# Kernel tuning notes

Measured on AMD Instinct MI355X. Metric: run time of the kernel, lower is better.

The kernel has to match this reference:

```python
import jax, jax.numpy as jnp
import numpy as np

B, N = 32, 512            # batch, max nodes per graph
F_DIM, M_DIM = 1024, 256  # node feature dim, first hidden dim
N_SEM = 8                 # number of semantic-class experts
XYZ, DIM_E = 3, 8
OUT_SIZE = 2 * XYZ + DIM_E  # 14 (default reg branch)
EPS = 1e-8                # padding value used by out_seq_to_batch


def setup_inputs() -> dict:
    key = jax.random.key(0)
    ks = jax.random.split(key, 12)
    def w(k, shape, fan_in):
        return jax.random.normal(k, shape, jnp.float32) / np.float32(np.sqrt(fan_in))
    return {
        "nodes": jax.random.normal(ks[0], (B, N, F_DIM), jnp.float32),
        "sem": jax.random.randint(ks[1], (B, N), 0, N_SEM, jnp.int32),
        "lengths": jax.random.randint(ks[2], (B,), 64, N + 1, jnp.int32),
        # y expert MLPs (4 layers), stacked over experts
        "W1": w(ks[3], (N_SEM, F_DIM, M_DIM), F_DIM), "b1": jnp.zeros((N_SEM, M_DIM), jnp.float32),
        "W2": w(ks[4], (N_SEM, M_DIM, 64), M_DIM),   "b2": jnp.zeros((N_SEM, 64), jnp.float32),
        "W3": w(ks[5], (N_SEM, 64, 32), 64),         "b3": jnp.zeros((N_SEM, 32), jnp.float32),
        "W4": w(ks[6], (N_SEM, 32, OUT_SIZE), 32),   "b4": jnp.zeros((N_SEM, OUT_SIZE), jnp.float32),
        # rot expert MLPs (2 layers), stacked over experts
        "R1": w(ks[7], (N_SEM, F_DIM, M_DIM), F_DIM), "rb1": jnp.zeros((N_SEM, M_DIM), jnp.float32),
        "R2": w(ks[8], (N_SEM, M_DIM, XYZ), M_DIM),   "rb2": jnp.zeros((N_SEM, XYZ), jnp.float32),
    }


def _prim_mlps(nodes, sem, lengths, W1, b1, W2, b2, W3, b3, W4, b4, R1, rb1, R2, rb2):
    Bn, Nn, Fd = nodes.shape
    x = nodes.reshape(-1, Fd)                       # [T, F], T = B*N tokens
    semf = sem.reshape(-1)                          # [T] expert id per token
    # dense dispatch: run every expert on all tokens, then select per token
    h1 = jax.nn.relu(jnp.einsum('tf,efm->etm', x, W1) + b1[:, None, :])   # [E,T,M]
    h2 = jax.nn.relu(jnp.einsum('etm,emh->eth', h1, W2) + b2[:, None, :]) # [E,T,64]
    h3 = jax.nn.relu(jnp.einsum('eth,ehg->etg', h2, W3) + b3[:, None, :]) # [E,T,32]
    y_all = jnp.einsum('etg,ego->eto', h3, W4) + b4[:, None, :]           # [E,T,OUT]
    r1 = jax.nn.relu(jnp.einsum('tf,efm->etm', x, R1) + rb1[:, None, :])  # [E,T,M]
    rot_all = jnp.einsum('etm,emo->eto', r1, R2) + rb2[:, None, :]        # [E,T,XYZ]
    t = jnp.arange(x.shape[0])
    y = y_all[semf, t]                              # [T, OUT]
    rot = rot_all[semf, t]                          # [T, XYZ]
    out = jnp.concatenate([y, rot], axis=-1).reshape(Bn, Nn, -1)
    # positions beyond each graph's length are filled with eps (out_seq_to_batch)
    mask = (jnp.arange(Nn)[None, :] < lengths[:, None])[:, :, None]
    return jnp.where(mask, out, jnp.float32(EPS))


def reference(nodes, sem, lengths, W1, b1, W2, b2, W3, b3, W4, b4, R1, rb1, R2, rb2):
    return _prim_mlps(nodes, sem, lengths, W1, b1, W2, b2, W3, b3, W4, b4,
                      R1, rb1, R2, rb2)
```

## Files before the change

kernel.cpp:

```cpp
#include <hip/hip_runtime.h>
#include <stdint.h>

#define T_TOK 16384
#define NE 8
#define EPSV 1e-8f
#define MAXC64  264
#define MAXC16  1032

#define WS_PERM   0
#define WS_PART   65536
#define WS_OFFS   67584
#define WS_XS     131072
#define WS_WT     (WS_XS + 16512*1024*2)
#define WS_H1     (WS_WT + 8*512*1024*2)
#define WS_W2T    (WS_H1 + 16448*512*2)
#define WS_W3T    (WS_W2T + 8*64*256*2)
#define WS_W4T    (WS_W3T + 8*32*64*2)
#define WS_R2T    (WS_W4T + 8*16*32*2)

typedef __attribute__((ext_vector_type(8))) short bf16x8;
typedef __attribute__((ext_vector_type(4))) float f32x4;

__device__ __forceinline__ unsigned short f2bf(float f) {
    unsigned u = __float_as_uint(f);
    u += 0x7fffu + ((u >> 16) & 1u);
    return (unsigned short)(u >> 16);
}

__device__ __forceinline__ void gl_lds16(const void* g, void* l) {
    __builtin_amdgcn_global_load_lds(
        (const __attribute__((address_space(1))) void*)g,
        (__attribute__((address_space(3))) void*)l,
        16, 0, 0);
}

__device__ __forceinline__ bool chunk_lookup(const int* __restrict__ offs, int c, int csize,
                                             int& e, int& base, int& len) {
    int acc = 0;
#pragma unroll
    for (int i = 0; i < NE; i++) {
        int s = offs[i], t = offs[i + 1];
        int cc = (t - s + csize - 1) / csize;
        if (c < acc + cc) {
            e = i;
            base = s + (c - acc) * csize;
            len = (t - base < csize) ? (t - base) : csize;
            return true;
        }
        acc += cc;
    }
    return false;
}

__global__ __launch_bounds__(256) void k_prep1(const float* __restrict__ W1,
                                               const float* __restrict__ R1,
                                               const float* __restrict__ W2,
                                               const float* __restrict__ W3,
                                               const float* __restrict__ W4,
                                               const float* __restrict__ R2,
                                               const int* __restrict__ sem,
                                               unsigned short* __restrict__ wt,
                                               unsigned short* __restrict__ w2t,
                                               unsigned short* __restrict__ w3t,
                                               unsigned short* __restrict__ w4t,
                                               unsigned short* __restrict__ r2t,
                                               int* __restrict__ ws_i) {
    __shared__ float tile[64][65];
    int id = blockIdx.x, tid = threadIdx.x;
    if (id >= 1024) {
        __shared__ int cnt[NE];
        int hb = id - 1024, lane = tid & 63;
        if (tid < NE) cnt[tid] = 0;
        __syncthreads();
        int s = sem[hb * 256 + tid];
#pragma unroll
        for (int e = 0; e < NE; e++) {
            unsigned long long m = __ballot(s == e);
            if (lane == e) atomicAdd(&cnt[e], (int)__popcll(m));
        }
        __syncthreads();
        if (tid < NE) ws_i[(WS_PART >> 2) + hb * NE + tid] = cnt[tid];
        return;
    }
    int e = id >> 7, rem = id & 127;
    int ny = rem >> 4, kx = rem & 15;
    int k0 = kx * 64, n0 = ny * 64;
    const float* src = (n0 < 256) ? (W1 + (size_t)e * 1024 * 256 + n0)
                                  : (R1 + (size_t)e * 1024 * 256 + (n0 - 256));
    int rr = tid >> 4;
    int cg = (tid & 15) * 4;
#pragma unroll
    for (int p = 0; p < 4; p++) {
        int kk = p * 16 + rr;
        float4 v = *(const float4*)(src + (size_t)(k0 + kk) * 256 + cg);
        tile[kk][cg] = v.x; tile[kk][cg + 1] = v.y; tile[kk][cg + 2] = v.z; tile[kk][cg + 3] = v.w;
    }
    __syncthreads();
    int nn = tid >> 3;
    int k8 = tid & 7;
#pragma unroll
    for (int p = 0; p < 2; p++) {
        int n = p * 32 + nn;
        unsigned w[4];
#pragma unroll
        for (int j = 0; j < 4; j++) {
            float f0 = tile[k8 * 8 + 2 * j][n];
            float f1 = tile[k8 * 8 + 2 * j + 1][n];
            w[j] = (unsigned)f2bf(f0) | ((unsigned)f2bf(f1) << 16);
        }
        *(uint4*)(wt + (size_t)(e * 512 + n0 + n) * 1024 + k0 + k8 * 8) =
            make_uint4(w[0], w[1], w[2], w[3]);
    }
    if (ny == 0) {
        int x = kx;
        for (int j = tid; j < 1024; j += 256) {
            int idx = x * 1024 + j; int k = idx & 255, n = idx >> 8;
            w2t[(size_t)(e * 64 + n) * 256 + k] = f2bf(W2[(size_t)e * 16384 + k * 64 + n]);
        }
        if (tid < 128) {
            int idx = x * 128 + tid; int k = idx & 63, n = idx >> 6;
            w3t[(size_t)(e * 32 + n) * 64 + k] = f2bf(W3[(size_t)e * 2048 + k * 32 + n]);
        }
        if (tid < 32) {
            int idx = x * 32 + tid; int k = idx & 31, n = idx >> 5;
            w4t[(size_t)(e * 16 + n) * 32 + k] = (n < 14) ? f2bf(W4[(size_t)e * 448 + k * 14 + n])
                                                          : (unsigned short)0;
        }
        {
            int idx = x * 256 + tid; int k = idx & 255, n = idx >> 8;
            r2t[(size_t)(e * 16 + n) * 256 + k] = (n < 3) ? f2bf(R2[(size_t)e * 768 + k * 3 + n])
                                                          : (unsigned short)0;
        }
    }
}

__global__ __launch_bounds__(256) void k_scatter(const int* __restrict__ sem,
                                                 const float* __restrict__ nodes,
                                                 int* __restrict__ ws_i,
                                                 unsigned short* __restrict__ xs) {
    __shared__ int parts[512];
    __shared__ int tot[NE], preb[NE], ebase[NE + 1];
    __shared__ int wcnt[4][NE];
    __shared__ int destS[256];
    int b = blockIdx.x, g = b >> 3, j = b & 7;
    int tid = threadIdx.x, wave = tid >> 6, lane = tid & 63;
    parts[tid] = ws_i[(WS_PART >> 2) + tid];
    parts[256 + tid] = ws_i[(WS_PART >> 2) + 256 + tid];
    __syncthreads();
    if (tid < NE) {
        int t = 0, p = 0;
        for (int bb = 0; bb < 64; bb++) {
            int v = parts[bb * NE + tid];
            t += v;
            if (bb < g) p += v;
        }
        tot[tid] = t; preb[tid] = p;
    }
    __syncthreads();
    if (tid == 0) {
        int base = 0;
        for (int e = 0; e < NE; e++) { ebase[e] = base; base += tot[e]; }
        ebase[NE] = base;
        if (b == 0)
            for (int e = 0; e <= NE; e++) ws_i[(WS_OFFS >> 2) + e] = ebase[e];
    }
    int i = g * 256 + tid;
    int s = sem[i];
    int rank = 0;
#pragma unroll
    for (int e = 0; e < NE; e++) {
        unsigned long long m = __ballot(s == e);
        if (s == e) rank = (int)__popcll(m & ((1ull << lane) - 1ull));
        if (lane == e) wcnt[wave][e] = (int)__popcll(m);
    }
    __syncthreads();
    int wpre = 0;
#pragma unroll
    for (int w = 0; w < 4; w++)
        if (w < wave) wpre += wcnt[w][s];
    int dest = ebase[s] + preb[s] + wpre + rank;
    destS[tid] = dest;
    if (j == 0) ws_i[(WS_PERM >> 2) + dest] = i;
    __syncthreads();
#pragma unroll 4
    for (int r = j * 32; r < j * 32 + 32; r++) {
        int tok = g * 256 + r;
        int d = destS[r];
        float4 v = *(const float4*)(nodes + (size_t)tok * 1024 + tid * 4);
        unsigned p0 = (unsigned)f2bf(v.x) | ((unsigned)f2bf(v.y) << 16);
        unsigned p1 = (unsigned)f2bf(v.z) | ((unsigned)f2bf(v.w) << 16);
        *(uint2*)(xs + (size_t)d * 1024 + tid * 4) = make_uint2(p0, p1);
    }
}

__global__ __launch_bounds__(256) void k_gemm(const unsigned short* __restrict__ xs,
                                              const unsigned short* __restrict__ wt,
                                              const float* __restrict__ b1,
                                              const float* __restrict__ rb1,
                                              const int* __restrict__ ws_i,
                                              unsigned short* __restrict__ h1) {
    __shared__ __align__(16) short As[2][64 * 64];
    __shared__ __align__(16) short Bs[2][128 * 64];
    int e, base, len;
    if (!chunk_lookup(ws_i + (WS_OFFS >> 2), blockIdx.x, 64, e, base, len)) return;
    int n0 = blockIdx.y * 128;
    int tid = threadIdx.x;
    int wave = tid >> 6, lane = tid & 63;
    int quad = lane >> 4, lr = lane & 15;
    int wn = wave * 32;

    f32x4 acc[4][2];
#pragma unroll
    for (int i = 0; i < 4; i++)
#pragma unroll
        for (int j = 0; j < 2; j++) acc[i][j] = (f32x4){0.f, 0.f, 0.f, 0.f};

    const unsigned short* Ag = xs + (size_t)base * 1024;
    const unsigned short* Bg = wt + (size_t)(e * 512 + n0) * 1024;

    const unsigned short* srcA[2];
    int dstA[2];
#pragma unroll
    for (int i = 0; i < 2; i++) {
        int s = i * 256 + wave * 64 + lane;
        int r = s >> 3, cs = (s & 7) ^ (r & 7);
        srcA[i] = Ag + (size_t)r * 1024 + cs * 8;
        dstA[i] = (i * 256 + wave * 64) * 8;
    }
    const unsigned short* srcB[4];
    int dstB[4];
#pragma unroll
    for (int i = 0; i < 4; i++) {
        int s = i * 256 + wave * 64 + lane;
        int r = s >> 3, cs = (s & 7) ^ (r & 7);
        srcB[i] = Bg + (size_t)r * 1024 + cs * 8;
        dstB[i] = (i * 256 + wave * 64) * 8;
    }

#pragma unroll
    for (int i = 0; i < 2; i++) gl_lds16(srcA[i], &As[0][dstA[i]]);
#pragma unroll
    for (int i = 0; i < 4; i++) gl_lds16(srcB[i], &Bs[0][dstB[i]]);

    for (int kb = 0; kb < 16; kb++) {
        int cur = kb & 1;
        if (kb < 15) {
            int nxt = cur ^ 1;
#pragma unroll
            for (int i = 0; i < 2; i++) gl_lds16(srcA[i] + (kb + 1) * 64, &As[nxt][dstA[i]]);
#pragma unroll
            for (int i = 0; i < 4; i++) gl_lds16(srcB[i] + (kb + 1) * 64, &Bs[nxt][dstB[i]]);
            asm volatile("s_waitcnt vmcnt(6)" ::: "memory");
        } else {
            asm volatile("s_waitcnt vmcnt(0)" ::: "memory");
        }
        __builtin_amdgcn_sched_barrier(0);
        __builtin_amdgcn_s_barrier();

        const short* Ab = As[cur];
        const short* Bb = Bs[cur];
        bf16x8 af[2][4], bfr[2][2];
#pragma unroll
        for (int im = 0; im < 4; im++) {
            int r = im * 16 + lr;
#pragma unroll
            for (int kh = 0; kh < 2; kh++) {
                int q = kh * 4 + quad;
                af[kh][im] = *(const bf16x8*)(Ab + (r * 8 + (q ^ (r & 7))) * 8);
            }
        }
#pragma unroll
        for (int in = 0; in < 2; in++) {
            int r = wn + in * 16 + lr;
#pragma unroll
            for (int kh = 0; kh < 2; kh++) {
                int q = kh * 4 + quad;
                bfr[kh][in] = *(const bf16x8*)(Bb + (r * 8 + (q ^ (r & 7))) * 8);
            }
        }
#pragma unroll
        for (int kh = 0; kh < 2; kh++)
#pragma unroll
            for (int im = 0; im < 4; im++)
#pragma unroll
                for (int in = 0; in < 2; in++)
                    acc[im][in] = __builtin_amdgcn_mfma_f32_16x16x32_bf16(af[kh][im], bfr[kh][in], acc[im][in], 0, 0, 0);

        if (kb < 15) {
            __builtin_amdgcn_sched_barrier(0);
            __builtin_amdgcn_s_barrier();
        }
    }

#pragma unroll
    for (int in = 0; in < 2; in++) {
        int gcol = n0 + wn + in * 16 + lr;
        float bias = (gcol < 256) ? b1[e * 256 + gcol] : rb1[e * 256 + gcol - 256];
#pragma unroll
        for (int im = 0; im < 4; im++) {
#pragma unroll
            for (int v = 0; v < 4; v++) {
                int r = im * 16 + quad * 4 + v;
                if (r < len) {
                    float val = fmaxf(acc[im][in][v] + bias, 0.f);
                    h1[(size_t)(base + r) * 512 + gcol] = f2bf(val);
                }
            }
        }
    }
}

__global__ __launch_bounds__(256) void k_tail(const unsigned short* __restrict__ h1,
                                              const int* __restrict__ ws_i,
                                              const unsigned short* __restrict__ w2t,
                                              const unsigned short* __restrict__ w3t,
                                              const unsigned short* __restrict__ w4t,
                                              const unsigned short* __restrict__ r2t,
                                              const float* __restrict__ b2,
                                              const float* __restrict__ b3,
                                              const float* __restrict__ b4,
                                              const float* __restrict__ rb2,
                                              const int* __restrict__ lengths,
                                              float* __restrict__ out) {
    __shared__ __align__(16) unsigned short h2s[16][64];
    __shared__ __align__(16) unsigned short h3s[16][32];

    int e, base, len;
    if (!chunk_lookup(ws_i + (WS_OFFS >> 2), blockIdx.x, 16, e, base, len)) return;
    int tid = threadIdx.x, wave = tid >> 6, lane = tid & 63;
    int quad = lane >> 4, lr = lane & 15;
    int lead = blockIdx.x & 3;

    const unsigned short* Ap = h1 + (size_t)base * 512;

    f32x4 acc2;
    { float bb = b2[e * 64 + wave * 16 + lr]; acc2 = (f32x4){bb, bb, bb, bb}; }
    f32x4 accr;
    { float bb = (lr < 3) ? rb2[e * 3 + lr] : 0.f; accr = (f32x4){bb, bb, bb, bb}; }

    const unsigned short* W2e = w2t + (size_t)e * 64 * 256;
    const unsigned short* R2e = r2t + (size_t)e * 16 * 256;
#pragma unroll
    for (int kk = 0; kk < 8; kk++) {
        int k0 = kk * 32;
        bf16x8 a = *(const bf16x8*)(Ap + lr * 512 + k0 + quad * 8);
        bf16x8 b = *(const bf16x8*)(W2e + (wave * 16 + lr) * 256 + k0 + quad * 8);
        acc2 = __builtin_amdgcn_mfma_f32_16x16x32_bf16(a, b, acc2, 0, 0, 0);
        if (wave == lead) {
            bf16x8 ar = *(const bf16x8*)(Ap + lr * 512 + 256 + k0 + quad * 8);
            bf16x8 br = *(const bf16x8*)(R2e + lr * 256 + k0 + quad * 8);
            accr = __builtin_amdgcn_mfma_f32_16x16x32_bf16(ar, br, accr, 0, 0, 0);
        }
    }
#pragma unroll
    for (int v = 0; v < 4; v++)
        h2s[quad * 4 + v][wave * 16 + lr] = f2bf(fmaxf(acc2[v], 0.f));
    __syncthreads();
    if (wave != lead) return;

    f32x4 acc3[2];
#pragma unroll
    for (int t = 0; t < 2; t++) {
        float bb = b3[e * 32 + t * 16 + lr];
        acc3[t] = (f32x4){bb, bb, bb, bb};
    }
    const unsigned short* W3e = w3t + (size_t)e * 32 * 64;
#pragma unroll
    for (int kk = 0; kk < 2; kk++) {
        int k0 = kk * 32;
        bf16x8 a = *(const bf16x8*)(&h2s[lr][k0 + quad * 8]);
#pragma unroll
        for (int t = 0; t < 2; t++) {
            bf16x8 b = *(const bf16x8*)(W3e + (t * 16 + lr) * 64 + k0 + quad * 8);
            acc3[t] = __builtin_amdgcn_mfma_f32_16x16x32_bf16(a, b, acc3[t], 0, 0, 0);
        }
    }
#pragma unroll
    for (int t = 0; t < 2; t++)
#pragma unroll
        for (int v = 0; v < 4; v++)
            h3s[quad * 4 + v][t * 16 + lr] = f2bf(fmaxf(acc3[t][v], 0.f));

    f32x4 acc4;
    { float bb = (lr < 14) ? b4[e * 14 + lr] : 0.f; acc4 = (f32x4){bb, bb, bb, bb}; }
    {
        bf16x8 a = *(const bf16x8*)(&h3s[lr][quad * 8]);
        bf16x8 b = *(const bf16x8*)(w4t + ((size_t)e * 16 + lr) * 32 + quad * 8);
        acc4 = __builtin_amdgcn_mfma_f32_16x16x32_bf16(a, b, acc4, 0, 0, 0);
    }

    const int* perm = ws_i + (WS_PERM >> 2);
#pragma unroll
    for (int v = 0; v < 4; v++) {
        int t = quad * 4 + v;
        if (t < len) {
            int token = perm[base + t];
            int bi = token >> 9, ni = token & 511;
            int valid = ni < lengths[bi];
            if (lr < 14) out[(size_t)token * 17 + lr] = valid ? acc4[v] : EPSV;
            if (lr < 3)  out[(size_t)token * 17 + 14 + lr] = valid ? accr[v] : EPSV;
        }
    }
}

extern "C" void kernel_launch(void* const* d_in, const int* in_sizes, int n_in,
                              void* d_out, int out_size, void* d_ws, size_t ws_size,
                              hipStream_t stream) {
    (void)in_sizes; (void)n_in; (void)out_size; (void)ws_size;
    const float* nodes   = (const float*)d_in[0];
    const int*   sem     = (const int*)d_in[1];
    const int*   lengths = (const int*)d_in[2];
    const float* W1 = (const float*)d_in[3];
    const float* b1 = (const float*)d_in[4];
    const float* W2 = (const float*)d_in[5];
    const float* b2 = (const float*)d_in[6];
    const float* W3 = (const float*)d_in[7];
    const float* b3 = (const float*)d_in[8];
    const float* W4 = (const float*)d_in[9];
    const float* b4 = (const float*)d_in[10];
    const float* R1  = (const float*)d_in[11];
    const float* rb1 = (const float*)d_in[12];
    const float* R2  = (const float*)d_in[13];
    const float* rb2 = (const float*)d_in[14];
    float* out = (float*)d_out;

    char* ws = (char*)d_ws;
    int* ws_i = (int*)ws;
    unsigned short* xs  = (unsigned short*)(ws + WS_XS);
    unsigned short* wt  = (unsigned short*)(ws + WS_WT);
    unsigned short* h1  = (unsigned short*)(ws + WS_H1);
    unsigned short* w2t = (unsigned short*)(ws + WS_W2T);
    unsigned short* w3t = (unsigned short*)(ws + WS_W3T);
    unsigned short* w4t = (unsigned short*)(ws + WS_W4T);
    unsigned short* r2t = (unsigned short*)(ws + WS_R2T);

    hipLaunchKernelGGL(k_prep1, dim3(1088), dim3(256), 0, stream,
                       W1, R1, W2, W3, W4, R2, sem, wt, w2t, w3t, w4t, r2t, ws_i);
    hipLaunchKernelGGL(k_scatter, dim3(512), dim3(256), 0, stream, sem, nodes, ws_i, xs);
    hipLaunchKernelGGL(k_gemm, dim3(MAXC64, 4), dim3(256), 0, stream,
                       (const unsigned short*)xs, (const unsigned short*)wt, b1, rb1,
                       (const int*)ws_i, h1);
    hipLaunchKernelGGL(k_tail, dim3(MAXC16), dim3(256), 0, stream,
                       (const unsigned short*)h1, (const int*)ws_i,
                       (const unsigned short*)w2t, (const unsigned short*)w3t,
                       (const unsigned short*)w4t, (const unsigned short*)r2t,
                       b2, b3, b4, rb2, lengths, out);
}
```

Baseline: 194.1 us.

## Fuse weight prep and token scatter into one kernel with redundant histograms

Merges the weight-transpose prep kernel and the token scatter kernel into a single launch. Each of the 512 scatter blocks now recomputes the global per-expert histogram and its block prefix by reading the whole sem array, so it no longer waits on a separate partial-count pass. This removes one kernel launch and the dependency between the two, letting weight conversion overlap with token scatter. The cost is redundant reads of sem (64 iterations per thread) and extra reduction work in every scatter block.

```diff
diff --git a/kernel.cpp b/kernel.cpp
--- a/kernel.cpp
+++ b/kernel.cpp
@@ -52,34 +52,85 @@
     return false;
 }
 
-__global__ __launch_bounds__(256) void k_prep1(const float* __restrict__ W1,
-                                               const float* __restrict__ R1,
-                                               const float* __restrict__ W2,
-                                               const float* __restrict__ W3,
-                                               const float* __restrict__ W4,
-                                               const float* __restrict__ R2,
-                                               const int* __restrict__ sem,
-                                               unsigned short* __restrict__ wt,
-                                               unsigned short* __restrict__ w2t,
-                                               unsigned short* __restrict__ w3t,
-                                               unsigned short* __restrict__ w4t,
-                                               unsigned short* __restrict__ r2t,
-                                               int* __restrict__ ws_i) {
+__global__ __launch_bounds__(256) void k_prep_scatter(const float* __restrict__ W1,
+                                                      const float* __restrict__ R1,
+                                                      const float* __restrict__ W2,
+                                                      const float* __restrict__ W3,
+                                                      const float* __restrict__ W4,
+                                                      const float* __restrict__ R2,
+                                                      const int* __restrict__ sem,
+                                                      const float* __restrict__ nodes,
+                                                      unsigned short* __restrict__ wt,
+                                                      unsigned short* __restrict__ w2t,
+                                                      unsigned short* __restrict__ w3t,
+                                                      unsigned short* __restrict__ w4t,
+                                                      unsigned short* __restrict__ r2t,
+                                                      unsigned short* __restrict__ xs,
+                                                      int* __restrict__ ws_i) {
     __shared__ float tile[64][65];
     int id = blockIdx.x, tid = threadIdx.x;
     if (id >= 1024) {
-        __shared__ int cnt[NE];
-        int hb = id - 1024, lane = tid & 63;
-        if (tid < NE) cnt[tid] = 0;
+        __shared__ int totS[NE], prebS[NE], ebase[NE + 1];
+        __shared__ int wcnt[4][NE];
+        __shared__ int destS[256];
+        int sb = id - 1024, g = sb >> 3, j = sb & 7;
+        int wave = tid >> 6, lane = tid & 63;
+
+        int ca[NE] = {0, 0, 0, 0, 0, 0, 0, 0};
+        int cp[NE] = {0, 0, 0, 0, 0, 0, 0, 0};
+        for (int i = 0; i < 64; i++) {
+            int s = sem[i * 256 + tid];
+#pragma unroll
+            for (int e = 0; e < NE; e++) {
+                int m = (s == e) ? 1 : 0;
+                ca[e] += m;
+                cp[e] += (i < g) ? m : 0;
+            }
+        }
+        if (tid < NE) { totS[tid] = 0; prebS[tid] = 0; }
         __syncthreads();
-        int s = sem[hb * 256 + tid];
+#pragma unroll
+        for (int e = 0; e < NE; e++) {
+            int v = ca[e], w = cp[e];
+#pragma unroll
+            for (int d = 1; d < 64; d <<= 1) { v += __shfl_xor(v, d); w += __shfl_xor(w, d); }
+            if (lane == 0) { atomicAdd(&totS[e], v); atomicAdd(&prebS[e], w); }
+        }
+        __syncthreads();
+        if (tid == 0) {
+            int b0 = 0;
+            for (int e = 0; e < NE; e++) { ebase[e] = b0; b0 += totS[e]; }
+            ebase[NE] = b0;
+            if (sb == 0)
+                for (int e = 0; e <= NE; e++) ws_i[(WS_OFFS >> 2) + e] = ebase[e];
+        }
+        int i = g * 256 + tid;
+        int s = sem[i];
+        int rank = 0;
 #pragma unroll
         for (int e = 0; e < NE; e++) {
             unsigned long long m = __ballot(s == e);
-            if (lane == e) atomicAdd(&cnt[e], (int)__popcll(m));
+            if (s == e) rank = (int)__popcll(m & ((1ull << lane) - 1ull));
+            if (lane == e) wcnt[wave][e] = (int)__popcll(m);
         }
         __syncthreads();
-        if (tid < NE) ws_i[(WS_PART >> 2) + hb * NE + tid] = cnt[tid];
+        int wpre = 0;
+#pragma unroll
+        for (int w = 0; w < 4; w++)
+            if (w < wave) wpre += wcnt[w][s];
+        int dest = ebase[s] + prebS[s] + wpre + rank;
+        destS[tid] = dest;
+        if (j == 0) ws_i[(WS_PERM >> 2) + dest] = i;
+        __syncthreads();
+#pragma unroll 4
+        for (int r = j * 32; r < j * 32 + 32; r++) {
+            int tok = g * 256 + r;
+            int d = destS[r];
+            float4 v = *(const float4*)(nodes + (size_t)tok * 1024 + tid * 4);
+            unsigned p0 = (unsigned)f2bf(v.x) | ((unsigned)f2bf(v.y) << 16);
+            unsigned p1 = (unsigned)f2bf(v.z) | ((unsigned)f2bf(v.w) << 16);
+            *(uint2*)(xs + (size_t)d * 1024 + tid * 4) = make_uint2(p0, p1);
+        }
         return;
     }
     int e = id >> 7, rem = id & 127;
@@ -131,65 +182,6 @@
             r2t[(size_t)(e * 16 + n) * 256 + k] = (n < 3) ? f2bf(R2[(size_t)e * 768 + k * 3 + n])
                                                           : (unsigned short)0;
         }
-    }
-}
-
-__global__ __launch_bounds__(256) void k_scatter(const int* __restrict__ sem,
-                                                 const float* __restrict__ nodes,
-                                                 int* __restrict__ ws_i,
-                                                 unsigned short* __restrict__ xs) {
-    __shared__ int parts[512];
-    __shared__ int tot[NE], preb[NE], ebase[NE + 1];
-    __shared__ int wcnt[4][NE];
-    __shared__ int destS[256];
-    int b = blockIdx.x, g = b >> 3, j = b & 7;
-    int tid = threadIdx.x, wave = tid >> 6, lane = tid & 63;
-    parts[tid] = ws_i[(WS_PART >> 2) + tid];
-    parts[256 + tid] = ws_i[(WS_PART >> 2) + 256 + tid];
-    __syncthreads();
-    if (tid < NE) {
-        int t = 0, p = 0;
-        for (int bb = 0; bb < 64; bb++) {
-            int v = parts[bb * NE + tid];
-            t += v;
-            if (bb < g) p += v;
-        }
-        tot[tid] = t; preb[tid] = p;
-    }
-    __syncthreads();
-    if (tid == 0) {
-        int base = 0;
-        for (int e = 0; e < NE; e++) { ebase[e] = base; base += tot[e]; }
-        ebase[NE] = base;
-        if (b == 0)
-            for (int e = 0; e <= NE; e++) ws_i[(WS_OFFS >> 2) + e] = ebase[e];
-    }
-    int i = g * 256 + tid;
-    int s = sem[i];
-    int rank = 0;
-#pragma unroll
-    for (int e = 0; e < NE; e++) {
-        unsigned long long m = __ballot(s == e);
-        if (s == e) rank = (int)__popcll(m & ((1ull << lane) - 1ull));
-        if (lane == e) wcnt[wave][e] = (int)__popcll(m);
-    }
-    __syncthreads();
-    int wpre = 0;
-#pragma unroll
-    for (int w = 0; w < 4; w++)
-        if (w < wave) wpre += wcnt[w][s];
-    int dest = ebase[s] + preb[s] + wpre + rank;
-    destS[tid] = dest;
-    if (j == 0) ws_i[(WS_PERM >> 2) + dest] = i;
-    __syncthreads();
-#pragma unroll 4
-    for (int r = j * 32; r < j * 32 + 32; r++) {
-        int tok = g * 256 + r;
-        int d = destS[r];
-        float4 v = *(const float4*)(nodes + (size_t)tok * 1024 + tid * 4);
-        unsigned p0 = (unsigned)f2bf(v.x) | ((unsigned)f2bf(v.y) << 16);
-        unsigned p1 = (unsigned)f2bf(v.z) | ((unsigned)f2bf(v.w) << 16);
-        *(uint2*)(xs + (size_t)d * 1024 + tid * 4) = make_uint2(p0, p1);
     }
 }
 
@@ -434,9 +426,9 @@
     unsigned short* w4t = (unsigned short*)(ws + WS_W4T);
     unsigned short* r2t = (unsigned short*)(ws + WS_R2T);
 
-    hipLaunchKernelGGL(k_prep1, dim3(1088), dim3(256), 0, stream,
-                       W1, R1, W2, W3, W4, R2, sem, wt, w2t, w3t, w4t, r2t, ws_i);
-    hipLaunchKernelGGL(k_scatter, dim3(512), dim3(256), 0, stream, sem, nodes, ws_i, xs);
+    hipLaunchKernelGGL(k_prep_scatter, dim3(1536), dim3(256), 0, stream,
+                       W1, R1, W2, W3, W4, R2, sem, nodes,
+                       wt, w2t, w3t, w4t, r2t, xs, ws_i);
     hipLaunchKernelGGL(k_gemm, dim3(MAXC64, 4), dim3(256), 0, stream,
                        (const unsigned short*)xs, (const unsigned short*)wt, b1, rb1,
                        (const int*)ws_i, h1);
```

New measurement: 199.4 us. +2.7%, slower.
